# Kernel tuning notes

Hardware: AMD Instinct MI355X
Metric: run time of the kernel (lower is better)

The kernel has to match this reference:

```python
import jax, jax.numpy as jnp
import numpy as np

TOKENS = 8192      # batch*seq flattened
D_IN = 2048        # in_features (power of 2 for Hadamard)
D_OUT = 8192       # out_features

try:
    FP8 = jnp.float8_e4m3fn
except AttributeError:
    FP8 = None


def fwht(x):
    """Normalized fast Walsh-Hadamard transform over last dim (power of 2)."""
    orig_shape = x.shape
    n = orig_shape[-1]
    x = x.reshape(-1, n)
    h = 1
    while h < n:
        x = x.reshape(-1, n // (2 * h), 2, h)
        a = x[..., 0, :]
        b = x[..., 1, :]
        x = jnp.stack([a + b, a - b], axis=-2).reshape(-1, n)
        h *= 2
    return (x * (1.0 / np.sqrt(n))).reshape(orig_shape)


def setup_inputs() -> dict:
    key = jax.random.key(0)
    kx, kw, kb = jax.random.split(key, 3)
    x = jax.random.normal(kx, (TOKENS, D_IN), dtype=jnp.float32)
    # Weight is stored in fp8 e4m3 (quantized in the Hadamard domain);
    # we materialize its dequantized fp32 values for the reference math.
    w = jax.random.normal(kw, (D_OUT, D_IN), dtype=jnp.float32) * 0.02
    if FP8 is not None:
        w = w.astype(FP8).astype(jnp.float32)  # simulate fp8 storage round-trip
    b = jax.random.normal(kb, (D_OUT,), dtype=jnp.float32) * 0.01
    return {"x": x, "weight": w, "bias": b}


def reference(x, weight, bias):
    # use_hadamard=True: rotate activations into the Hadamard domain
    # (weight was quantized in that domain), then fp8-dequant GEMM + bias.
    x_h = fwht(x)                               # [T, D_IN]
    out = jnp.einsum('td,od->to', x_h, weight)  # [T, D_OUT]
    return out + bias[None, :]
```

## Files before the change

### kernel.cpp

```cpp
#include <hip/hip_runtime.h>
#include <hip/hip_bf16.h>
#include <stdint.h>

#define TOKENS 8192
#define D_IN   2048
#define D_OUT  8192

typedef __attribute__((ext_vector_type(8))) short short8;
typedef __attribute__((ext_vector_type(4))) float floatx4;

__device__ __forceinline__ void async_copy16(const void* g, void* l) {
    __builtin_amdgcn_global_load_lds((const __attribute__((address_space(1))) void*)g,
                                     (__attribute__((address_space(3))) void*)l,
                                     16, 0, 0);
}

__device__ __forceinline__ void fwht8(float* e) {
#pragma unroll
    for (int s = 1; s < 8; s <<= 1) {
#pragma unroll
        for (int j = 0; j < 8; ++j) {
            if ((j & s) == 0) {
                float a = e[j], b = e[j | s];
                e[j]     = a + b;
                e[j | s] = a - b;
            }
        }
    }
}

__global__ __launch_bounds__(256) void fwht_kernel(const float* __restrict__ x,
                                                   __hip_bfloat16* __restrict__ xh) {
    __shared__ float row[D_IN];
    const int r = blockIdx.x;
    const int t = threadIdx.x;
    const float* xr = x + (size_t)r * D_IN;

    float e[8];
#pragma unroll
    for (int j = 0; j < 8; ++j) e[j] = xr[t + 256 * j];
    fwht8(e);
#pragma unroll
    for (int j = 0; j < 8; ++j) row[t + 256 * j] = e[j];
    __syncthreads();

    float f[8];
#pragma unroll
    for (int j = 0; j < 8; ++j) f[j] = row[8 * t + j];
    fwht8(f);
#pragma unroll
    for (int m = 1; m <= 16; m <<= 1) {
#pragma unroll
        for (int j = 0; j < 8; ++j) {
            float v = __shfl_xor(f[j], m, 64);
            f[j] = (t & m) ? (v - f[j]) : (f[j] + v);
        }
    }

    const float scale = 0.02209708691207961f;
    __hip_bfloat16 ob[8];
#pragma unroll
    for (int j = 0; j < 8; ++j) ob[j] = __float2bfloat16(f[j] * scale);
    __hip_bfloat16* orow = xh + (size_t)r * D_IN + 8 * t;
    *reinterpret_cast<int4*>(orow) = *reinterpret_cast<int4*>(ob);
}

__global__ __launch_bounds__(256) void wconv_kernel(const float* __restrict__ w,
                                                    __hip_bfloat16* __restrict__ wb) {
    const size_t i = ((size_t)blockIdx.x * 256 + threadIdx.x) * 8;
    float4 a = *reinterpret_cast<const float4*>(w + i);
    float4 b = *reinterpret_cast<const float4*>(w + i + 4);
    __hip_bfloat16 ob[8];
    ob[0] = __float2bfloat16(a.x); ob[1] = __float2bfloat16(a.y);
    ob[2] = __float2bfloat16(a.z); ob[3] = __float2bfloat16(a.w);
    ob[4] = __float2bfloat16(b.x); ob[5] = __float2bfloat16(b.y);
    ob[6] = __float2bfloat16(b.z); ob[7] = __float2bfloat16(b.w);
    *reinterpret_cast<int4*>(wb + i) = *reinterpret_cast<int4*>(ob);
}

__global__ __launch_bounds__(256) void gemm_kernel(const __hip_bfloat16* __restrict__ A,
                                                   const __hip_bfloat16* __restrict__ B,
                                                   const float* __restrict__ bias,
                                                   float* __restrict__ C) {
    __shared__ __hip_bfloat16 sA[128 * 32];
    __shared__ __hip_bfloat16 sB[128 * 32];

    const int tid  = threadIdx.x;
    const int wave = tid >> 6;
    const int lane = tid & 63;
    const int bm = blockIdx.y;
    const int bn = blockIdx.x;

    const int wm = wave & 1;
    const int wn = wave >> 1;
    const int lane16 = lane & 15;
    const int lgrp   = lane >> 4;

    floatx4 acc[4][4];
#pragma unroll
    for (int i = 0; i < 4; ++i)
#pragma unroll
        for (int j = 0; j < 4; ++j) acc[i][j] = 0;

    const int c0 = (wave * 2 + 0) * 64 + lane;
    const int c1 = (wave * 2 + 1) * 64 + lane;
    const int rA0 = c0 >> 2, kc0 = c0 & 3;
    const int rA1 = c1 >> 2, kc1 = c1 & 3;

    const __hip_bfloat16* gA0 = A + (size_t)(bm * 128 + rA0) * D_IN + kc0 * 8;
    const __hip_bfloat16* gA1 = A + (size_t)(bm * 128 + rA1) * D_IN + kc1 * 8;
    const __hip_bfloat16* gB0 = B + (size_t)(bn * 128 + rA0) * D_IN + kc0 * 8;
    const __hip_bfloat16* gB1 = B + (size_t)(bn * 128 + rA1) * D_IN + kc1 * 8;
    __hip_bfloat16* lA0 = sA + c0 * 8;
    __hip_bfloat16* lA1 = sA + c1 * 8;
    __hip_bfloat16* lB0 = sB + c0 * 8;
    __hip_bfloat16* lB1 = sB + c1 * 8;

    for (int k0 = 0; k0 < D_IN; k0 += 32) {
        async_copy16(gA0 + k0, lA0);
        async_copy16(gA1 + k0, lA1);
        async_copy16(gB0 + k0, lB0);
        async_copy16(gB1 + k0, lB1);
        __syncthreads();

        short8 af[4], bf[4];
#pragma unroll
        for (int i = 0; i < 4; ++i) {
            af[i] = *reinterpret_cast<const short8*>(sA + (wm * 64 + i * 16 + lane16) * 32 + lgrp * 8);
            bf[i] = *reinterpret_cast<const short8*>(sB + (wn * 64 + i * 16 + lane16) * 32 + lgrp * 8);
        }
#pragma unroll
        for (int i = 0; i < 4; ++i)
#pragma unroll
            for (int j = 0; j < 4; ++j)
                acc[i][j] = __builtin_amdgcn_mfma_f32_16x16x32_bf16(af[i], bf[j], acc[i][j], 0, 0, 0);
        __syncthreads();
    }

    float bv[4];
#pragma unroll
    for (int j = 0; j < 4; ++j) bv[j] = bias[bn * 128 + wn * 64 + j * 16 + lane16];

#pragma unroll
    for (int i = 0; i < 4; ++i) {
        const int rbase = bm * 128 + wm * 64 + i * 16 + lgrp * 4;
#pragma unroll
        for (int j = 0; j < 4; ++j) {
            const int col = bn * 128 + wn * 64 + j * 16 + lane16;
#pragma unroll
            for (int r = 0; r < 4; ++r) {
                C[(size_t)(rbase + r) * D_OUT + col] = acc[i][j][r] + bv[j];
            }
        }
    }
}

extern "C" void kernel_launch(void* const* d_in, const int* in_sizes, int n_in,
                              void* d_out, int out_size, void* d_ws, size_t ws_size,
                              hipStream_t stream) {
    const float* x    = (const float*)d_in[0];
    const float* w    = (const float*)d_in[1];
    const float* bias = (const float*)d_in[2];
    float* out = (float*)d_out;

    __hip_bfloat16* xh = (__hip_bfloat16*)d_ws;
    __hip_bfloat16* wb = xh + (size_t)TOKENS * D_IN;

    fwht_kernel<<<TOKENS, 256, 0, stream>>>(x, xh);
    wconv_kernel<<<(D_OUT * D_IN / 8) / 256, 256, 0, stream>>>(w, wb);
    gemm_kernel<<<dim3(D_OUT / 128, TOKENS / 128), 256, 0, stream>>>(xh, wb, bias, out);
}
```

Baseline: 647.0 us.

## Rewrite GEMM with 256x256 tiles, double-buffered async LDS loads, and swizzling

Replaces the 128x128 single-buffered bf16 GEMM with a 512-thread, 256x256-tile kernel. It double-buffers BK=64 K-slices in 128KB of dynamic LDS and interleaves async global-to-LDS stages with MFMA phases, using barriers and s_setprio. It also adds an XOR swizzle to avoid LDS bank conflicts and remaps block IDs for L2 locality. This targets the per-iteration load-then-compute serialization and low arithmetic intensity of the old kernel, at the cost of heavy register and LDS use and fragile hand-written vmcnt synchronization.

```diff
diff --git a/kernel.cpp b/kernel.cpp
--- a/kernel.cpp
+++ b/kernel.cpp
@@ -5,6 +5,8 @@
 #define TOKENS 8192
 #define D_IN   2048
 #define D_OUT  8192
+#define BK     64
+#define NT     (D_IN / BK)
 
 typedef __attribute__((ext_vector_type(8))) short short8;
 typedef __attribute__((ext_vector_type(4))) float floatx4;
@@ -78,78 +80,168 @@
     *reinterpret_cast<int4*>(wb + i) = *reinterpret_cast<int4*>(ob);
 }
 
-__global__ __launch_bounds__(256) void gemm_kernel(const __hip_bfloat16* __restrict__ A,
-                                                   const __hip_bfloat16* __restrict__ B,
-                                                   const float* __restrict__ bias,
-                                                   float* __restrict__ C) {
-    __shared__ __hip_bfloat16 sA[128 * 32];
-    __shared__ __hip_bfloat16 sB[128 * 32];
-
-    const int tid  = threadIdx.x;
-    const int wave = tid >> 6;
-    const int lane = tid & 63;
-    const int bm = blockIdx.y;
-    const int bn = blockIdx.x;
-
-    const int wm = wave & 1;
-    const int wn = wave >> 1;
+__global__ __launch_bounds__(512, 2) void gemm_kernel(const __hip_bfloat16* __restrict__ A,
+                                                      const __hip_bfloat16* __restrict__ B,
+                                                      const float* __restrict__ bias,
+                                                      float* __restrict__ C) {
+    extern __shared__ float4 smem_f4[];
+    __hip_bfloat16* sA = (__hip_bfloat16*)smem_f4;
+    __hip_bfloat16* sB = sA + 2 * 16384;
+
+    const int tid    = threadIdx.x;
+    const int wave   = tid >> 6;
+    const int lane   = tid & 63;
     const int lane16 = lane & 15;
     const int lgrp   = lane >> 4;
 
-    floatx4 acc[4][4];
-#pragma unroll
-    for (int i = 0; i < 4; ++i)
-#pragma unroll
-        for (int j = 0; j < 4; ++j) acc[i][j] = 0;
-
-    const int c0 = (wave * 2 + 0) * 64 + lane;
-    const int c1 = (wave * 2 + 1) * 64 + lane;
-    const int rA0 = c0 >> 2, kc0 = c0 & 3;
-    const int rA1 = c1 >> 2, kc1 = c1 & 3;
-
-    const __hip_bfloat16* gA0 = A + (size_t)(bm * 128 + rA0) * D_IN + kc0 * 8;
-    const __hip_bfloat16* gA1 = A + (size_t)(bm * 128 + rA1) * D_IN + kc1 * 8;
-    const __hip_bfloat16* gB0 = B + (size_t)(bn * 128 + rA0) * D_IN + kc0 * 8;
-    const __hip_bfloat16* gB1 = B + (size_t)(bn * 128 + rA1) * D_IN + kc1 * 8;
-    __hip_bfloat16* lA0 = sA + c0 * 8;
-    __hip_bfloat16* lA1 = sA + c1 * 8;
-    __hip_bfloat16* lB0 = sB + c0 * 8;
-    __hip_bfloat16* lB1 = sB + c1 * 8;
-
-    for (int k0 = 0; k0 < D_IN; k0 += 32) {
-        async_copy16(gA0 + k0, lA0);
-        async_copy16(gA1 + k0, lA1);
-        async_copy16(gB0 + k0, lB0);
-        async_copy16(gB1 + k0, lB1);
-        __syncthreads();
-
-        short8 af[4], bf[4];
-#pragma unroll
-        for (int i = 0; i < 4; ++i) {
-            af[i] = *reinterpret_cast<const short8*>(sA + (wm * 64 + i * 16 + lane16) * 32 + lgrp * 8);
-            bf[i] = *reinterpret_cast<const short8*>(sB + (wn * 64 + i * 16 + lane16) * 32 + lgrp * 8);
-        }
-#pragma unroll
-        for (int i = 0; i < 4; ++i)
-#pragma unroll
-            for (int j = 0; j < 4; ++j)
-                acc[i][j] = __builtin_amdgcn_mfma_f32_16x16x32_bf16(af[i], bf[j], acc[i][j], 0, 0, 0);
-        __syncthreads();
+    const int bid = blockIdx.x;
+    const int s   = (bid & 7) * 128 + (bid >> 3);
+    const int bm  = s >> 5;
+    const int bn  = s & 31;
+
+    const int wm = wave >> 2;
+    const int wn = wave & 3;
+
+    const int srow = lane >> 3;
+    const int scc8 = ((lane & 7) ^ srow) * 8;
+    const int r0   = wave * 16 + srow;
+    const __hip_bfloat16* gAst = A + (size_t)(bm * 256) * D_IN + scc8;
+    const __hip_bfloat16* gBst = B + (size_t)(bn * 256) * D_IN + scc8;
+
+    auto stageA = [&](int kt, int h) {
+        const __hip_bfloat16* g = gAst + (size_t)(h * 128 + r0) * D_IN + kt * BK;
+        __hip_bfloat16* l = sA + (kt & 1) * 16384 + h * 8192 + wave * 1024;
+        async_copy16(g, l);
+        async_copy16(g + (size_t)8 * D_IN, l + 512);
+    };
+    auto stageB = [&](int kt, int h) {
+        const __hip_bfloat16* g = gBst + (size_t)(h * 128 + r0) * D_IN + kt * BK;
+        __hip_bfloat16* l = sB + (kt & 1) * 16384 + h * 8192 + wave * 1024;
+        async_copy16(g, l);
+        async_copy16(g + (size_t)8 * D_IN, l + 512);
+    };
+
+    const int sw   = lane16 & 7;
+    const int cK0  = ((0 + lgrp) ^ sw) * 8;
+    const int cK1  = ((4 + lgrp) ^ sw) * 8;
+    const int arow = wm * 128 + lane16;
+    const int brow = wn * 64  + lane16;
+
+    floatx4 acc[8][4];
+#pragma unroll
+    for (int m = 0; m < 8; ++m)
+#pragma unroll
+        for (int n = 0; n < 4; ++n) acc[m][n] = 0;
+
+    stageA(0, 0); stageA(0, 1);
+    stageB(0, 0); stageB(0, 1);
+    stageA(1, 0); stageA(1, 1);
+    asm volatile("s_waitcnt vmcnt(4)" ::: "memory");
+    asm volatile("s_barrier" ::: "memory");
+
+    short8 af[8][2];
+    short8 bf[4][2];
+
+#pragma unroll 2
+    for (int kt = 0; kt < NT; ++kt) {
+        const __hip_bfloat16* aB = sA + ((kt & 1) << 14);
+        const __hip_bfloat16* bB = sB + ((kt & 1) << 14);
+
+#pragma unroll
+        for (int m = 0; m < 4; ++m) {
+            const __hip_bfloat16* p = aB + (arow + m * 16) * 64;
+            af[m][0] = *reinterpret_cast<const short8*>(p + cK0);
+            af[m][1] = *reinterpret_cast<const short8*>(p + cK1);
+        }
+#pragma unroll
+        for (int n = 0; n < 2; ++n) {
+            const __hip_bfloat16* p = bB + (brow + n * 16) * 64;
+            bf[n][0] = *reinterpret_cast<const short8*>(p + cK0);
+            bf[n][1] = *reinterpret_cast<const short8*>(p + cK1);
+        }
+        if (kt + 1 < NT) stageB(kt + 1, 0);
+        asm volatile("s_barrier" ::: "memory");
+        __builtin_amdgcn_s_setprio(1);
+#pragma unroll
+        for (int m = 0; m < 4; ++m)
+#pragma unroll
+            for (int n = 0; n < 2; ++n) {
+                acc[m][n] = __builtin_amdgcn_mfma_f32_16x16x32_bf16(af[m][0], bf[n][0], acc[m][n], 0, 0, 0);
+                acc[m][n] = __builtin_amdgcn_mfma_f32_16x16x32_bf16(af[m][1], bf[n][1], acc[m][n], 0, 0, 0);
+            }
+        __builtin_amdgcn_s_setprio(0);
+        asm volatile("s_barrier" ::: "memory");
+
+#pragma unroll
+        for (int m = 4; m < 8; ++m) {
+            const __hip_bfloat16* p = aB + (arow + m * 16) * 64;
+            af[m][0] = *reinterpret_cast<const short8*>(p + cK0);
+            af[m][1] = *reinterpret_cast<const short8*>(p + cK1);
+        }
+        if (kt + 1 < NT) stageB(kt + 1, 1);
+        asm volatile("s_barrier" ::: "memory");
+        __builtin_amdgcn_s_setprio(1);
+#pragma unroll
+        for (int m = 4; m < 8; ++m)
+#pragma unroll
+            for (int n = 0; n < 2; ++n) {
+                acc[m][n] = __builtin_amdgcn_mfma_f32_16x16x32_bf16(af[m][0], bf[n][0], acc[m][n], 0, 0, 0);
+                acc[m][n] = __builtin_amdgcn_mfma_f32_16x16x32_bf16(af[m][1], bf[n][1], acc[m][n], 0, 0, 0);
+            }
+        __builtin_amdgcn_s_setprio(0);
+        asm volatile("s_barrier" ::: "memory");
+
+#pragma unroll
+        for (int n = 2; n < 4; ++n) {
+            const __hip_bfloat16* p = bB + (brow + n * 16) * 64;
+            bf[n][0] = *reinterpret_cast<const short8*>(p + cK0);
+            bf[n][1] = *reinterpret_cast<const short8*>(p + cK1);
+        }
+        if (kt + 2 < NT) stageA(kt + 2, 0);
+        asm volatile("s_barrier" ::: "memory");
+        __builtin_amdgcn_s_setprio(1);
+#pragma unroll
+        for (int m = 0; m < 4; ++m)
+#pragma unroll
+            for (int n = 2; n < 4; ++n) {
+                acc[m][n] = __builtin_amdgcn_mfma_f32_16x16x32_bf16(af[m][0], bf[n][0], acc[m][n], 0, 0, 0);
+                acc[m][n] = __builtin_amdgcn_mfma_f32_16x16x32_bf16(af[m][1], bf[n][1], acc[m][n], 0, 0, 0);
+            }
+        __builtin_amdgcn_s_setprio(0);
+        asm volatile("s_barrier" ::: "memory");
+
+        if (kt + 2 < NT) stageA(kt + 2, 1);
+        asm volatile("s_barrier" ::: "memory");
+        __builtin_amdgcn_s_setprio(1);
+#pragma unroll
+        for (int m = 4; m < 8; ++m)
+#pragma unroll
+            for (int n = 2; n < 4; ++n) {
+                acc[m][n] = __builtin_amdgcn_mfma_f32_16x16x32_bf16(af[m][0], bf[n][0], acc[m][n], 0, 0, 0);
+                acc[m][n] = __builtin_amdgcn_mfma_f32_16x16x32_bf16(af[m][1], bf[n][1], acc[m][n], 0, 0, 0);
+            }
+        __builtin_amdgcn_s_setprio(0);
+        if (kt + 2 < NT) {
+            asm volatile("s_waitcnt vmcnt(4)" ::: "memory");
+        } else {
+            asm volatile("s_waitcnt vmcnt(0)" ::: "memory");
+        }
+        asm volatile("s_barrier" ::: "memory");
     }
 
     float bv[4];
 #pragma unroll
-    for (int j = 0; j < 4; ++j) bv[j] = bias[bn * 128 + wn * 64 + j * 16 + lane16];
-
-#pragma unroll
-    for (int i = 0; i < 4; ++i) {
-        const int rbase = bm * 128 + wm * 64 + i * 16 + lgrp * 4;
-#pragma unroll
-        for (int j = 0; j < 4; ++j) {
-            const int col = bn * 128 + wn * 64 + j * 16 + lane16;
+    for (int n = 0; n < 4; ++n) bv[n] = bias[bn * 256 + wn * 64 + n * 16 + lane16];
+
+#pragma unroll
+    for (int m = 0; m < 8; ++m) {
+        const int rbase = bm * 256 + wm * 128 + m * 16 + lgrp * 4;
+#pragma unroll
+        for (int n = 0; n < 4; ++n) {
+            const int col = bn * 256 + wn * 64 + n * 16 + lane16;
 #pragma unroll
             for (int r = 0; r < 4; ++r) {
-                C[(size_t)(rbase + r) * D_OUT + col] = acc[i][j][r] + bv[j];
+                C[(size_t)(rbase + r) * D_OUT + col] = acc[m][n][r] + bv[n];
             }
         }
     }
@@ -166,7 +258,14 @@
     __hip_bfloat16* xh = (__hip_bfloat16*)d_ws;
     __hip_bfloat16* wb = xh + (size_t)TOKENS * D_IN;
 
+    static bool attr_set = false;
+    if (!attr_set) {
+        (void)hipFuncSetAttribute((const void*)gemm_kernel,
+                                  hipFuncAttributeMaxDynamicSharedMemorySize, 131072);
+        attr_set = true;
+    }
+
     fwht_kernel<<<TOKENS, 256, 0, stream>>>(x, xh);
     wconv_kernel<<<(D_OUT * D_IN / 8) / 256, 256, 0, stream>>>(w, wb);
-    gemm_kernel<<<dim3(D_OUT / 128, TOKENS / 128), 256, 0, stream>>>(xh, wb, bias, out);
-}
+    gemm_kernel<<<1024, 512, 131072, stream>>>(xh, wb, bias, out);
+}
```

After: 568.7 us. 12.1% less time.
